# Performance work log

Hardware: AMD Instinct MI355X
Metric: run time of the kernel (lower is better)

## Reference

```python
import jax, jax.numpy as jnp
import numpy as np

B, L, S, H, E, D = 2, 2048, 2048, 16, 64, 64


def setup_inputs() -> dict:
    key = jax.random.key(0)
    ks = jax.random.split(key, 6)
    return {
        "q1": jax.random.normal(ks[0], (B, L, H, E), dtype=jnp.float32),
        "k1": jax.random.normal(ks[1], (B, S, H, E), dtype=jnp.float32),
        "v1": jax.random.normal(ks[2], (B, S, H, D), dtype=jnp.float32),
        "q2": jax.random.normal(ks[3], (B, L, H, E), dtype=jnp.float32),
        "k2": jax.random.normal(ks[4], (B, S, H, E), dtype=jnp.float32),
        "v2": jax.random.normal(ks[5], (B, S, H, D), dtype=jnp.float32),
        "attn_mask": 0,  # accepted but unused by the original forward
    }


def reference(q1, k1, v1, q2, k2, v2, attn_mask):
    # scale = 1/sqrt(E) (self.scale is None in init_kwargs)
    scale = 1.0 / jnp.sqrt(jnp.asarray(q1.shape[-1], dtype=q1.dtype))
    # dual QK scores: [B,H,L,S]
    scores1 = jnp.einsum('blhe,bshe->bhls', q1, k1)
    scores2 = jnp.einsum('blhe,bshe->bhls', q2, k2)
    # eval-mode (dropout disabled for deterministic reference)
    A = jnp.tanh(scores1 * scale) * jax.nn.sigmoid(scores2 * scale)
    # weighted V matmul: [B,L,H,D]
    out = jnp.einsum('bhls,bshd->blhd', A, v1)
    return out
```

## Files before the change

kernel.cpp:

```cpp
#include <hip/hip_runtime.h>

constexpr int Bc = 2, Lc = 2048, Sc = 2048, Hc = 16, Ec = 64, Dc = 64;
constexpr int TILES = Sc / 64;
constexpr int NBH   = Bc * Hc;
constexpr size_t TILE_ELEMS = 4096;
constexpr size_t ARR_ELEMS  = (size_t)NBH * TILES * TILE_ELEMS;
constexpr size_t WS_NEED    = ARR_ELEMS * 2 * 3;

typedef float          f32x4  __attribute__((ext_vector_type(4)));
typedef __bf16         bf16x8 __attribute__((ext_vector_type(8)));
typedef unsigned short u16x8  __attribute__((ext_vector_type(8)));
typedef unsigned short u16x4  __attribute__((ext_vector_type(4)));
typedef unsigned int   u32x4  __attribute__((ext_vector_type(4)));

static __device__ __forceinline__ unsigned cvtpk(float lo, float hi) {
    unsigned r;
    asm("v_cvt_pk_bf16_f32 %0, %1, %2" : "=v"(r) : "v"(lo), "v"(hi));
    return r;
}

static __device__ __forceinline__ void gl2lds16(const void* g, void* l) {
    __builtin_amdgcn_global_load_lds(
        (const __attribute__((address_space(1))) unsigned int*)g,
        (__attribute__((address_space(3))) unsigned int*)l, 16, 0, 0);
}

static __device__ __forceinline__ float fexp2(float x) {
#if __has_builtin(__builtin_amdgcn_exp2f)
    return __builtin_amdgcn_exp2f(x);
#else
    return exp2f(x);
#endif
}

__global__ __launch_bounds__(256) void prepass_kernel(
    const float* __restrict__ k1, const float* __restrict__ k2,
    const float* __restrict__ v1,
    unsigned short* __restrict__ k1b, unsigned short* __restrict__ k2b,
    unsigned short* __restrict__ vb)
{
    __shared__ unsigned short vt[64 * 80];

    const int blk = blockIdx.x;
    const int st  = blk & 31;
    const int bh  = blk >> 5;
    const int b   = bh >> 4, h = bh & 15;
    const int s0  = st * 64;
    const size_t tileo = (size_t)blk * TILE_ELEMS;

    #pragma unroll
    for (int it = 0; it < 2; ++it) {
        int u  = threadIdx.x + it * 256;
        int s  = u >> 3, e8 = u & 7;
        size_t g = ((size_t)((b * Sc + s0 + s) * Hc + h)) * Ec + e8 * 8;

        float4 x0 = *reinterpret_cast<const float4*>(k1 + g);
        float4 x1 = *reinterpret_cast<const float4*>(k1 + g + 4);
        u32x4 o;
        o[0] = cvtpk(x0.x, x0.y); o[1] = cvtpk(x0.z, x0.w);
        o[2] = cvtpk(x1.x, x1.y); o[3] = cvtpk(x1.z, x1.w);
        *reinterpret_cast<u32x4*>(&k1b[tileo + (size_t)(s * 8 + (e8 ^ (s & 7))) * 8]) = o;

        x0 = *reinterpret_cast<const float4*>(k2 + g);
        x1 = *reinterpret_cast<const float4*>(k2 + g + 4);
        o[0] = cvtpk(x0.x, x0.y); o[1] = cvtpk(x0.z, x0.w);
        o[2] = cvtpk(x1.x, x1.y); o[3] = cvtpk(x1.z, x1.w);
        *reinterpret_cast<u32x4*>(&k2b[tileo + (size_t)(s * 8 + (e8 ^ (s & 7))) * 8]) = o;

        x0 = *reinterpret_cast<const float4*>(v1 + g);
        x1 = *reinterpret_cast<const float4*>(v1 + g + 4);
        o[0] = cvtpk(x0.x, x0.y); o[1] = cvtpk(x0.z, x0.w);
        o[2] = cvtpk(x1.x, x1.y); o[3] = cvtpk(x1.z, x1.w);
        *reinterpret_cast<u32x4*>(&vt[s * 80 + e8 * 8]) = o;
    }
    __syncthreads();

    #pragma unroll
    for (int it = 0; it < 2; ++it) {
        int u  = threadIdx.x + it * 256;
        int d  = u >> 3, sc8 = u & 7;
        u16x8 o;
        #pragma unroll
        for (int j = 0; j < 8; ++j) o[j] = vt[(sc8 * 8 + j) * 80 + d];
        *reinterpret_cast<u16x8*>(&vb[tileo + (size_t)(d * 8 + (sc8 ^ (d & 7))) * 8]) = o;
    }
}

__global__ __launch_bounds__(256) void fused_kernel(
    const float* __restrict__ q1, const float* __restrict__ q2,
    const unsigned short* __restrict__ k1b, const unsigned short* __restrict__ k2b,
    const unsigned short* __restrict__ vb, float* __restrict__ out)
{
    __shared__ unsigned short k1t[4096];
    __shared__ unsigned short k2t[4096];
    __shared__ unsigned short vtt[4096];
    __shared__ unsigned int   ptb[4][608];

    const int orig    = blockIdx.x;
    const int logical = (orig & 7) * 128 + (orig >> 3);
    const int lblk = logical & 31;
    const int bh   = logical >> 5;
    const int b    = bh >> 4, h = bh & 15;

    const int tid  = threadIdx.x;
    const int w    = tid >> 6;
    const int lane = tid & 63;
    const int lr   = lane & 15;
    const int lg   = lane >> 4;

    constexpr float C1 = 0.36067376022224085f;
    constexpr float C2 = -0.18033688011112043f;
    const int    qrow  = lblk * 64 + w * 16 + lr;
    const size_t qbase = ((size_t)((b * Lc + qrow) * Hc + h)) * Ec;
    bf16x8 a1[2], a2[2];
    #pragma unroll
    for (int es = 0; es < 2; ++es) {
        const float* p1 = q1 + qbase + es * 32 + lg * 8;
        const float* p2 = q2 + qbase + es * 32 + lg * 8;
        float4 x0 = *reinterpret_cast<const float4*>(p1);
        float4 x1 = *reinterpret_cast<const float4*>(p1 + 4);
        u32x4 o;
        o[0] = cvtpk(x0.x * C1, x0.y * C1); o[1] = cvtpk(x0.z * C1, x0.w * C1);
        o[2] = cvtpk(x1.x * C1, x1.y * C1); o[3] = cvtpk(x1.z * C1, x1.w * C1);
        a1[es] = __builtin_bit_cast(bf16x8, o);
        x0 = *reinterpret_cast<const float4*>(p2);
        x1 = *reinterpret_cast<const float4*>(p2 + 4);
        o[0] = cvtpk(x0.x * C2, x0.y * C2); o[1] = cvtpk(x0.z * C2, x0.w * C2);
        o[2] = cvtpk(x1.x * C2, x1.y * C2); o[3] = cvtpk(x1.z * C2, x1.w * C2);
        a2[es] = __builtin_bit_cast(bf16x8, o);
    }

    f32x4 acc[4];
    #pragma unroll
    for (int i = 0; i < 4; ++i) acc[i] = (f32x4){0.f, 0.f, 0.f, 0.f};

    const unsigned short* k1g = k1b + (size_t)bh * TILES * TILE_ELEMS;
    const unsigned short* k2g = k2b + (size_t)bh * TILES * TILE_ELEMS;
    const unsigned short* vg  = vb  + (size_t)bh * TILES * TILE_ELEMS;
    unsigned int* ptw = &ptb[w][0];

    for (int st = 0; st < TILES; ++st) {
        const size_t tb = (size_t)st * TILE_ELEMS + tid * 8;
        gl2lds16(k1g + tb,        &k1t[tid * 8]);
        gl2lds16(k1g + tb + 2048, &k1t[2048 + tid * 8]);
        gl2lds16(k2g + tb,        &k2t[tid * 8]);
        gl2lds16(k2g + tb + 2048, &k2t[2048 + tid * 8]);
        gl2lds16(vg  + tb,        &vtt[tid * 8]);
        gl2lds16(vg  + tb + 2048, &vtt[2048 + tid * 8]);
        __syncthreads();

        #pragma unroll
        for (int ct = 0; ct < 4; ++ct) {
            f32x4 s1 = {0.f, 0.f, 0.f, 0.f}, s2 = {0.f, 0.f, 0.f, 0.f};
            #pragma unroll
            for (int es = 0; es < 2; ++es) {
                const int off = (ct * 16 + lr) * 64 + (((4 * es + lg) ^ (lr & 7)) * 8);
                bf16x8 kb1 = __builtin_bit_cast(bf16x8, *reinterpret_cast<const u16x8*>(&k1t[off]));
                bf16x8 kb2 = __builtin_bit_cast(bf16x8, *reinterpret_cast<const u16x8*>(&k2t[off]));
                s1 = __builtin_amdgcn_mfma_f32_16x16x32_bf16(kb1, a1[es], s1, 0, 0, 0);
                s2 = __builtin_amdgcn_mfma_f32_16x16x32_bf16(kb2, a2[es], s2, 0, 0, 0);
            }
            float p[4];
            #pragma unroll
            for (int i = 0; i < 4; ++i) {
                float t  = fexp2(s1[i]);
                float uu = fexp2(s2[i]);
                p[i] = (t - 1.f) * __builtin_amdgcn_rcpf((t + 1.f) * (1.f + uu));
            }
            const int pb = (8 * ct + 2 * lg) * 19 + lr;
            ptw[pb]      = cvtpk(p[0], p[1]);
            ptw[pb + 19] = cvtpk(p[2], p[3]);
        }

        #pragma unroll
        for (int ks = 0; ks < 2; ++ks) {
            u32x4 pw;
            #pragma unroll
            for (int wd = 0; wd < 4; ++wd)
                pw[wd] = ptw[(16 * ks + 4 * lg + wd) * 19 + lr];
            bf16x8 pa = __builtin_bit_cast(bf16x8, pw);
            #pragma unroll
            for (int dt = 0; dt < 4; ++dt) {
                const int off = (dt * 16 + lr) * 64 + (((4 * ks + lg) ^ (lr & 7)) * 8);
                bf16x8 vf = __builtin_bit_cast(bf16x8, *reinterpret_cast<const u16x8*>(&vtt[off]));
                acc[dt] = __builtin_amdgcn_mfma_f32_16x16x32_bf16(pa, vf, acc[dt], 0, 0, 0);
            }
        }
        __syncthreads();
    }

    const int orow = lblk * 64 + w * 16;
    #pragma unroll
    for (int dt = 0; dt < 4; ++dt)
        #pragma unroll
        for (int i = 0; i < 4; ++i) {
            int l = orow + lg * 4 + i;
            out[((size_t)(b * Lc + l) * Hc + h) * Dc + dt * 16 + lr] = acc[dt][i];
        }
}

static __device__ __forceinline__ unsigned short f2bf(float f) {
    unsigned u = __builtin_bit_cast(unsigned, f);
    u += 0x7fffu + ((u >> 16) & 1u);
    return (unsigned short)(u >> 16);
}

__global__ __launch_bounds__(256) void fallback_kernel(
    const float* __restrict__ q1, const float* __restrict__ k1,
    const float* __restrict__ v1, const float* __restrict__ q2,
    const float* __restrict__ k2, float* __restrict__ out)
{
    constexpr int KSTR = 72, VSTR = 88, PSTR = 88;
    __shared__ unsigned short k1t[64 * KSTR];
    __shared__ unsigned short k2t[64 * KSTR];
    __shared__ unsigned short vtt[64 * VSTR];
    __shared__ unsigned short pt [4 * 16 * PSTR];

    const int blk  = blockIdx.x;
    const int lblk = blk & 31;
    const int bh   = blk >> 5;
    const int b    = bh >> 4;
    const int h    = bh & 15;
    const int tid  = threadIdx.x;
    const int w    = tid >> 6;
    const int lane = tid & 63;
    const int lr   = lane & 15;
    const int lg   = lane >> 4;

    const int    qrow  = lblk * 64 + w * 16 + lr;
    const size_t qbase = ((size_t)(b * Lc + qrow) * Hc + h) * Ec;
    bf16x8 a1[2], a2[2];
    for (int es = 0; es < 2; ++es) {
        u16x8 t1, t2;
        for (int j = 0; j < 8; ++j) {
            t1[j] = f2bf(q1[qbase + es * 32 + lg * 8 + j]);
            t2[j] = f2bf(q2[qbase + es * 32 + lg * 8 + j]);
        }
        a1[es] = __builtin_bit_cast(bf16x8, t1);
        a2[es] = __builtin_bit_cast(bf16x8, t2);
    }
    f32x4 acc[4];
    for (int i = 0; i < 4; ++i) acc[i] = (f32x4){0.f, 0.f, 0.f, 0.f};
    constexpr float CT = 0.25f, CS = -0.125f;

    for (int s0 = 0; s0 < Sc; s0 += 64) {
        for (int it = 0; it < 4; ++it) {
            int idx = tid + it * 256;
            int sr  = idx >> 4;
            int c4  = (idx & 15) << 2;
            size_t gk = ((size_t)(b * Sc + s0 + sr) * Hc + h) * Ec + c4;
            float4 x1 = *reinterpret_cast<const float4*>(k1 + gk);
            float4 x2 = *reinterpret_cast<const float4*>(k2 + gk);
            float4 xv = *reinterpret_cast<const float4*>(v1 + gk);
            u16x4 o1, o2;
            o1[0]=f2bf(x1.x); o1[1]=f2bf(x1.y); o1[2]=f2bf(x1.z); o1[3]=f2bf(x1.w);
            o2[0]=f2bf(x2.x); o2[1]=f2bf(x2.y); o2[2]=f2bf(x2.z); o2[3]=f2bf(x2.w);
            *reinterpret_cast<u16x4*>(&k1t[sr * KSTR + c4]) = o1;
            *reinterpret_cast<u16x4*>(&k2t[sr * KSTR + c4]) = o2;
            vtt[(c4 + 0) * VSTR + sr] = f2bf(xv.x);
            vtt[(c4 + 1) * VSTR + sr] = f2bf(xv.y);
            vtt[(c4 + 2) * VSTR + sr] = f2bf(xv.z);
            vtt[(c4 + 3) * VSTR + sr] = f2bf(xv.w);
        }
        __syncthreads();
        for (int ct = 0; ct < 4; ++ct) {
            f32x4 s1 = {0.f,0.f,0.f,0.f}, s2 = {0.f,0.f,0.f,0.f};
            for (int es = 0; es < 2; ++es) {
                bf16x8 b1 = __builtin_bit_cast(bf16x8,
                    *reinterpret_cast<const u16x8*>(&k1t[(ct*16 + lr) * KSTR + es*32 + lg*8]));
                bf16x8 b2 = __builtin_bit_cast(bf16x8,
                    *reinterpret_cast<const u16x8*>(&k2t[(ct*16 + lr) * KSTR + es*32 + lg*8]));
                s1 = __builtin_amdgcn_mfma_f32_16x16x32_bf16(a1[es], b1, s1, 0, 0, 0);
                s2 = __builtin_amdgcn_mfma_f32_16x16x32_bf16(a2[es], b2, s2, 0, 0, 0);
            }
            for (int i = 0; i < 4; ++i) {
                float xa = fminf(fmaxf(s1[i] * CT, -30.f), 30.f);
                float xb = fminf(fmaxf(s2[i] * CS, -30.f), 30.f);
                float t  = __expf(xa);
                float u  = __expf(xb);
                float p  = (t - 1.f) * __builtin_amdgcn_rcpf((t + 1.f) * (1.f + u));
                pt[(w*16 + lg*4 + i) * PSTR + ct*16 + lr] = f2bf(p);
            }
        }
        asm volatile("s_waitcnt lgkmcnt(0)" ::: "memory");
        for (int ks = 0; ks < 2; ++ks) {
            bf16x8 pa = __builtin_bit_cast(bf16x8,
                *reinterpret_cast<const u16x8*>(&pt[(w*16 + lr) * PSTR + ks*32 + lg*8]));
            for (int dt = 0; dt < 4; ++dt) {
                bf16x8 vf = __builtin_bit_cast(bf16x8,
                    *reinterpret_cast<const u16x8*>(&vtt[(dt*16 + lr) * VSTR + ks*32 + lg*8]));
                acc[dt] = __builtin_amdgcn_mfma_f32_16x16x32_bf16(pa, vf, acc[dt], 0, 0, 0);
            }
        }
        __syncthreads();
    }
    const int orow = lblk * 64 + w * 16;
    for (int dt = 0; dt < 4; ++dt)
        for (int i = 0; i < 4; ++i) {
            int l = orow + lg * 4 + i;
            out[((size_t)(b * Lc + l) * Hc + h) * Dc + dt * 16 + lr] = acc[dt][i];
        }
}

extern "C" void kernel_launch(void* const* d_in, const int* in_sizes, int n_in,
                              void* d_out, int out_size, void* d_ws, size_t ws_size,
                              hipStream_t stream) {
    const float* q1 = (const float*)d_in[0];
    const float* k1 = (const float*)d_in[1];
    const float* v1 = (const float*)d_in[2];
    const float* q2 = (const float*)d_in[3];
    const float* k2 = (const float*)d_in[4];
    float* out = (float*)d_out;

    if (ws_size >= WS_NEED) {
        unsigned short* k1b = (unsigned short*)d_ws;
        unsigned short* k2b = k1b + ARR_ELEMS;
        unsigned short* vbp = k2b + ARR_ELEMS;
        prepass_kernel<<<dim3(NBH * TILES), dim3(256), 0, stream>>>(k1, k2, v1, k1b, k2b, vbp);
        fused_kernel<<<dim3(NBH * TILES), dim3(256), 0, stream>>>(q1, q2, k1b, k2b, vbp, out);
    } else {
        fallback_kernel<<<dim3(NBH * TILES), dim3(256), 0, stream>>>(q1, k1, v1, q2, k2, out);
    }
}
```

Before: 117.4 us.

## Split key tile across warp pairs, double-buffer K in LDS, load V directly

Reorganizes the fused attention kernel so each pair of warps shares a 32-row query group, with each warp handling half of the 64-key tile and producing two 16-row query blocks. K1/K2 tiles are double-buffered in LDS with a prefetch of the next tile, while V fragments are read straight from global memory in an unswizzled layout. A small per-warp LDS bounce buffer converts P to the A-operand layout, and partial outputs from the two halves are reduced through LDS at the end. The goals are to overlap loads with compute, reuse each K fragment across two query blocks, and cut LDS footprint to allow more occupancy. The cost is more register pressure and uncached global V reads on every iteration.

```diff
diff --git a/kernel.cpp b/kernel.cpp
--- a/kernel.cpp
+++ b/kernel.cpp
@@ -12,6 +12,7 @@
 typedef unsigned short u16x8  __attribute__((ext_vector_type(8)));
 typedef unsigned short u16x4  __attribute__((ext_vector_type(4)));
 typedef unsigned int   u32x4  __attribute__((ext_vector_type(4)));
+typedef unsigned int   u32x2  __attribute__((ext_vector_type(2)));
 
 static __device__ __forceinline__ unsigned cvtpk(float lo, float hi) {
     unsigned r;
@@ -82,19 +83,17 @@
         u16x8 o;
         #pragma unroll
         for (int j = 0; j < 8; ++j) o[j] = vt[(sc8 * 8 + j) * 80 + d];
-        *reinterpret_cast<u16x8*>(&vb[tileo + (size_t)(d * 8 + (sc8 ^ (d & 7))) * 8]) = o;
-    }
-}
-
-__global__ __launch_bounds__(256) void fused_kernel(
+        *reinterpret_cast<u16x8*>(&vb[tileo + (size_t)(d * 8 + sc8) * 8]) = o;
+    }
+}
+
+__global__ __launch_bounds__(256, 4) void fused_kernel(
     const float* __restrict__ q1, const float* __restrict__ q2,
     const unsigned short* __restrict__ k1b, const unsigned short* __restrict__ k2b,
     const unsigned short* __restrict__ vb, float* __restrict__ out)
 {
-    __shared__ unsigned short k1t[4096];
-    __shared__ unsigned short k2t[4096];
-    __shared__ unsigned short vtt[4096];
-    __shared__ unsigned int   ptb[4][608];
+    __shared__ unsigned short klds[2][2][4096];
+    __shared__ unsigned int   pbounce[4][256];
 
     const int orig    = blockIdx.x;
     const int logical = (orig & 7) * 128 + (orig >> 3);
@@ -107,96 +106,156 @@
     const int lane = tid & 63;
     const int lr   = lane & 15;
     const int lg   = lane >> 4;
+    const int qsub = w >> 1;
+    const int sh   = w & 1;
 
     constexpr float C1 = 0.36067376022224085f;
     constexpr float C2 = -0.18033688011112043f;
-    const int    qrow  = lblk * 64 + w * 16 + lr;
-    const size_t qbase = ((size_t)((b * Lc + qrow) * Hc + h)) * Ec;
-    bf16x8 a1[2], a2[2];
+    bf16x8 a1[2][2], a2[2][2];
     #pragma unroll
-    for (int es = 0; es < 2; ++es) {
-        const float* p1 = q1 + qbase + es * 32 + lg * 8;
-        const float* p2 = q2 + qbase + es * 32 + lg * 8;
-        float4 x0 = *reinterpret_cast<const float4*>(p1);
-        float4 x1 = *reinterpret_cast<const float4*>(p1 + 4);
-        u32x4 o;
-        o[0] = cvtpk(x0.x * C1, x0.y * C1); o[1] = cvtpk(x0.z * C1, x0.w * C1);
-        o[2] = cvtpk(x1.x * C1, x1.y * C1); o[3] = cvtpk(x1.z * C1, x1.w * C1);
-        a1[es] = __builtin_bit_cast(bf16x8, o);
-        x0 = *reinterpret_cast<const float4*>(p2);
-        x1 = *reinterpret_cast<const float4*>(p2 + 4);
-        o[0] = cvtpk(x0.x * C2, x0.y * C2); o[1] = cvtpk(x0.z * C2, x0.w * C2);
-        o[2] = cvtpk(x1.x * C2, x1.y * C2); o[3] = cvtpk(x1.z * C2, x1.w * C2);
-        a2[es] = __builtin_bit_cast(bf16x8, o);
-    }
-
-    f32x4 acc[4];
+    for (int qg = 0; qg < 2; ++qg) {
+        const int    qrow  = lblk * 64 + qsub * 32 + qg * 16 + lr;
+        const size_t qbase = ((size_t)((b * Lc + qrow) * Hc + h)) * Ec;
+        #pragma unroll
+        for (int es = 0; es < 2; ++es) {
+            const float* p1 = q1 + qbase + es * 32 + lg * 8;
+            const float* p2 = q2 + qbase + es * 32 + lg * 8;
+            float4 x0 = *reinterpret_cast<const float4*>(p1);
+            float4 x1 = *reinterpret_cast<const float4*>(p1 + 4);
+            u32x4 o;
+            o[0] = cvtpk(x0.x * C1, x0.y * C1); o[1] = cvtpk(x0.z * C1, x0.w * C1);
+            o[2] = cvtpk(x1.x * C1, x1.y * C1); o[3] = cvtpk(x1.z * C1, x1.w * C1);
+            a1[qg][es] = __builtin_bit_cast(bf16x8, o);
+            x0 = *reinterpret_cast<const float4*>(p2);
+            x1 = *reinterpret_cast<const float4*>(p2 + 4);
+            o[0] = cvtpk(x0.x * C2, x0.y * C2); o[1] = cvtpk(x0.z * C2, x0.w * C2);
+            o[2] = cvtpk(x1.x * C2, x1.y * C2); o[3] = cvtpk(x1.z * C2, x1.w * C2);
+            a2[qg][es] = __builtin_bit_cast(bf16x8, o);
+        }
+    }
+
+    f32x4 acc[2][4];
     #pragma unroll
-    for (int i = 0; i < 4; ++i) acc[i] = (f32x4){0.f, 0.f, 0.f, 0.f};
+    for (int qg = 0; qg < 2; ++qg)
+        #pragma unroll
+        for (int dt = 0; dt < 4; ++dt) acc[qg][dt] = (f32x4){0.f, 0.f, 0.f, 0.f};
 
     const unsigned short* k1g = k1b + (size_t)bh * TILES * TILE_ELEMS;
     const unsigned short* k2g = k2b + (size_t)bh * TILES * TILE_ELEMS;
     const unsigned short* vg  = vb  + (size_t)bh * TILES * TILE_ELEMS;
-    unsigned int* ptw = &ptb[w][0];
-
+    unsigned int* pb = &pbounce[w][0];
+
+    {
+        const size_t tb = (size_t)tid * 8;
+        gl2lds16(k1g + tb,        &klds[0][0][tid * 8]);
+        gl2lds16(k1g + tb + 2048, &klds[0][0][tid * 8 + 2048]);
+        gl2lds16(k2g + tb,        &klds[0][1][tid * 8]);
+        gl2lds16(k2g + tb + 2048, &klds[0][1][tid * 8 + 2048]);
+    }
+
+    int cur = 0;
     for (int st = 0; st < TILES; ++st) {
-        const size_t tb = (size_t)st * TILE_ELEMS + tid * 8;
-        gl2lds16(k1g + tb,        &k1t[tid * 8]);
-        gl2lds16(k1g + tb + 2048, &k1t[2048 + tid * 8]);
-        gl2lds16(k2g + tb,        &k2t[tid * 8]);
-        gl2lds16(k2g + tb + 2048, &k2t[2048 + tid * 8]);
-        gl2lds16(vg  + tb,        &vtt[tid * 8]);
-        gl2lds16(vg  + tb + 2048, &vtt[2048 + tid * 8]);
         __syncthreads();
-
-        #pragma unroll
-        for (int ct = 0; ct < 4; ++ct) {
-            f32x4 s1 = {0.f, 0.f, 0.f, 0.f}, s2 = {0.f, 0.f, 0.f, 0.f};
+        if (st + 1 < TILES) {
+            const size_t tb = (size_t)(st + 1) * TILE_ELEMS + tid * 8;
+            const int nxt = cur ^ 1;
+            gl2lds16(k1g + tb,        &klds[nxt][0][tid * 8]);
+            gl2lds16(k1g + tb + 2048, &klds[nxt][0][tid * 8 + 2048]);
+            gl2lds16(k2g + tb,        &klds[nxt][1][tid * 8]);
+            gl2lds16(k2g + tb + 2048, &klds[nxt][1][tid * 8 + 2048]);
+        }
+
+        unsigned pq1[4];
+        #pragma unroll
+        for (int c = 0; c < 2; ++c) {
+            f32x4 s1[2] = {{0.f,0.f,0.f,0.f},{0.f,0.f,0.f,0.f}};
+            f32x4 s2[2] = {{0.f,0.f,0.f,0.f},{0.f,0.f,0.f,0.f}};
             #pragma unroll
             for (int es = 0; es < 2; ++es) {
-                const int off = (ct * 16 + lr) * 64 + (((4 * es + lg) ^ (lr & 7)) * 8);
-                bf16x8 kb1 = __builtin_bit_cast(bf16x8, *reinterpret_cast<const u16x8*>(&k1t[off]));
-                bf16x8 kb2 = __builtin_bit_cast(bf16x8, *reinterpret_cast<const u16x8*>(&k2t[off]));
-                s1 = __builtin_amdgcn_mfma_f32_16x16x32_bf16(kb1, a1[es], s1, 0, 0, 0);
-                s2 = __builtin_amdgcn_mfma_f32_16x16x32_bf16(kb2, a2[es], s2, 0, 0, 0);
-            }
-            float p[4];
+                const int off = ((sh * 2 + c) * 16 + lr) * 64 + (((4 * es + lg) ^ (lr & 7)) * 8);
+                bf16x8 kb1 = __builtin_bit_cast(bf16x8, *reinterpret_cast<const u16x8*>(&klds[cur][0][off]));
+                bf16x8 kb2 = __builtin_bit_cast(bf16x8, *reinterpret_cast<const u16x8*>(&klds[cur][1][off]));
+                #pragma unroll
+                for (int qg = 0; qg < 2; ++qg) {
+                    s1[qg] = __builtin_amdgcn_mfma_f32_16x16x32_bf16(kb1, a1[qg][es], s1[qg], 0, 0, 0);
+                    s2[qg] = __builtin_amdgcn_mfma_f32_16x16x32_bf16(kb2, a2[qg][es], s2[qg], 0, 0, 0);
+                }
+            }
             #pragma unroll
-            for (int i = 0; i < 4; ++i) {
-                float t  = fexp2(s1[i]);
-                float uu = fexp2(s2[i]);
-                p[i] = (t - 1.f) * __builtin_amdgcn_rcpf((t + 1.f) * (1.f + uu));
-            }
-            const int pb = (8 * ct + 2 * lg) * 19 + lr;
-            ptw[pb]      = cvtpk(p[0], p[1]);
-            ptw[pb + 19] = cvtpk(p[2], p[3]);
-        }
-
-        #pragma unroll
-        for (int ks = 0; ks < 2; ++ks) {
-            u32x4 pw;
+            for (int qg = 0; qg < 2; ++qg) {
+                float p[4];
+                #pragma unroll
+                for (int i = 0; i < 4; ++i) {
+                    float t  = fexp2(s1[qg][i]);
+                    float uu = fexp2(s2[qg][i]);
+                    p[i] = (t - 1.f) * __builtin_amdgcn_rcpf((t + 1.f) * (1.f + uu));
+                }
+                unsigned w0 = cvtpk(p[0], p[1]);
+                unsigned w1 = cvtpk(p[2], p[3]);
+                if (qg == 0) {
+                    *reinterpret_cast<u32x2*>(&pb[(c * 4 + lg) * 32 + 2 * lr]) = (u32x2){w0, w1};
+                } else {
+                    pq1[c * 2] = w0; pq1[c * 2 + 1] = w1;
+                }
+            }
+        }
+
+        u16x8 vfr[4];
+        #pragma unroll
+        for (int dt = 0; dt < 4; ++dt)
+            vfr[dt] = *reinterpret_cast<const u16x8*>(
+                &vg[(size_t)st * TILE_ELEMS + (dt * 16 + lr) * 64 + sh * 32 + lg * 8]);
+
+        asm volatile("" ::: "memory");
+        u32x2 r0 = *reinterpret_cast<const u32x2*>(&pb[(2 * lg) * 32 + 2 * lr]);
+        u32x2 r1 = *reinterpret_cast<const u32x2*>(&pb[(2 * lg + 1) * 32 + 2 * lr]);
+        bf16x8 pa0 = __builtin_bit_cast(bf16x8, (u32x4){r0[0], r0[1], r1[0], r1[1]});
+        #pragma unroll
+        for (int dt = 0; dt < 4; ++dt)
+            acc[0][dt] = __builtin_amdgcn_mfma_f32_16x16x32_bf16(
+                pa0, __builtin_bit_cast(bf16x8, vfr[dt]), acc[0][dt], 0, 0, 0);
+
+        asm volatile("" ::: "memory");
+        *reinterpret_cast<u32x2*>(&pb[(lg) * 32 + 2 * lr])     = (u32x2){pq1[0], pq1[1]};
+        *reinterpret_cast<u32x2*>(&pb[(4 + lg) * 32 + 2 * lr]) = (u32x2){pq1[2], pq1[3]};
+        asm volatile("" ::: "memory");
+        r0 = *reinterpret_cast<const u32x2*>(&pb[(2 * lg) * 32 + 2 * lr]);
+        r1 = *reinterpret_cast<const u32x2*>(&pb[(2 * lg + 1) * 32 + 2 * lr]);
+        bf16x8 pa1 = __builtin_bit_cast(bf16x8, (u32x4){r0[0], r0[1], r1[0], r1[1]});
+        #pragma unroll
+        for (int dt = 0; dt < 4; ++dt)
+            acc[1][dt] = __builtin_amdgcn_mfma_f32_16x16x32_bf16(
+                pa1, __builtin_bit_cast(bf16x8, vfr[dt]), acc[1][dt], 0, 0, 0);
+
+        cur ^= 1;
+    }
+
+    __syncthreads();
+    float* mbuf = reinterpret_cast<float*>(&klds[0][0][0]);
+    if (sh == 1) {
+        #pragma unroll
+        for (int qg = 0; qg < 2; ++qg)
             #pragma unroll
-            for (int wd = 0; wd < 4; ++wd)
-                pw[wd] = ptw[(16 * ks + 4 * lg + wd) * 19 + lr];
-            bf16x8 pa = __builtin_bit_cast(bf16x8, pw);
+            for (int dt = 0; dt < 4; ++dt)
+                *reinterpret_cast<f32x4*>(&mbuf[(((qsub * 2 + qg) * 4 + dt) * 256) + lane * 4]) = acc[qg][dt];
+    }
+    __syncthreads();
+    if (sh == 0) {
+        #pragma unroll
+        for (int qg = 0; qg < 2; ++qg) {
+            const int orow = lblk * 64 + qsub * 32 + qg * 16;
             #pragma unroll
             for (int dt = 0; dt < 4; ++dt) {
-                const int off = (dt * 16 + lr) * 64 + (((4 * ks + lg) ^ (lr & 7)) * 8);
-                bf16x8 vf = __builtin_bit_cast(bf16x8, *reinterpret_cast<const u16x8*>(&vtt[off]));
-                acc[dt] = __builtin_amdgcn_mfma_f32_16x16x32_bf16(pa, vf, acc[dt], 0, 0, 0);
-            }
-        }
-        __syncthreads();
-    }
-
-    const int orow = lblk * 64 + w * 16;
-    #pragma unroll
-    for (int dt = 0; dt < 4; ++dt)
-        #pragma unroll
-        for (int i = 0; i < 4; ++i) {
-            int l = orow + lg * 4 + i;
-            out[((size_t)(b * Lc + l) * Hc + h) * Dc + dt * 16 + lr] = acc[dt][i];
-        }
+                f32x4 o = *reinterpret_cast<const f32x4*>(&mbuf[(((qsub * 2 + qg) * 4 + dt) * 256) + lane * 4]);
+                o += acc[qg][dt];
+                #pragma unroll
+                for (int i = 0; i < 4; ++i) {
+                    int l = orow + lg * 4 + i;
+                    out[((size_t)(b * Lc + l) * Hc + h) * Dc + dt * 16 + lr] = o[i];
+                }
+            }
+        }
+    }
 }
 
 static __device__ __forceinline__ unsigned short f2bf(float f) {
```

Measured after the change: 115.3 us. About the same (-1.8%).
